# Performance work log

Hardware: AMD Instinct MI355X
Metric: run time of the kernel (lower is better)

The kernel has to match this reference:

```python
import jax, jax.numpy as jnp
import numpy as np

DIM = 1024
HEADS = 8
HEAD_DIM = DIM // HEADS
TAU = HEAD_DIM ** 0.5
BS, SEQ = 1, 2048


def setup_inputs() -> dict:
    key = jax.random.key(0)
    kq, kk, kv, kb = jax.random.split(key, 4)
    q = jax.random.normal(kq, (BS, SEQ, DIM), jnp.float32)
    k = jax.random.normal(kk, (BS, SEQ, DIM), jnp.float32)
    v = jax.random.normal(kv, (BS, SEQ, DIM), jnp.float32)
    Wi_w = jnp.zeros((HEADS, 3 * DIM), jnp.float32)
    Wi_b = 0.1 * jax.random.normal(kb, (HEADS,), jnp.float32)
    Wf_w = jnp.zeros((HEADS, 3 * DIM), jnp.float32)
    Wf_b = jnp.linspace(3.0, 6.0, HEADS, dtype=jnp.float32)  # equidistant_bias_init(3, 6)
    gn_w = jnp.ones((DIM,), jnp.float32)
    gn_b = jnp.zeros((DIM,), jnp.float32)
    return {"q": q, "k": k, "v": v, "Wi_w": Wi_w, "Wi_b": Wi_b,
            "Wf_w": Wf_w, "Wf_b": Wf_b, "gn_w": gn_w, "gn_b": gn_b}


def reference(q, k, v, Wi_w, Wi_b, Wf_w, Wf_b, gn_w, gn_b):
    bs, seq, dim = q.shape
    gate_in = jnp.concatenate([q, k, v], axis=-1)                    # [b, s, 3d]
    itilde = jnp.einsum('bsd,hd->bhs', gate_in, Wi_w) + Wi_b[None, :, None]
    ftilde = jnp.einsum('bsd,hd->bhs', gate_in, Wf_w) + Wf_b[None, :, None]

    # Decay matrix: F_act[i,j] = sum_{t=j+1..i} logsigmoid(ftilde_t), lower-tri else -inf
    csum = jnp.cumsum(jax.nn.log_sigmoid(ftilde), axis=-1)           # [b, h, s]
    Fmat = csum[..., :, None] - csum[..., None, :]                   # [b, h, s, s]
    mask = jnp.tril(jnp.ones((seq, seq), dtype=bool))
    F_act = jnp.where(mask, Fmat, -jnp.inf)

    Dtilde = F_act + itilde[..., None, :]                            # add input gate along j
    max_d = jnp.max(Dtilde, axis=-1, keepdims=True)
    D = jnp.exp(Dtilde - max_d)                                      # stabilized decay weights

    qh = q.reshape(bs, seq, HEADS, HEAD_DIM).transpose(0, 2, 1, 3)
    kh = k.reshape(bs, seq, HEADS, HEAD_DIM).transpose(0, 2, 1, 3)
    vh = v.reshape(bs, seq, HEADS, HEAD_DIM).transpose(0, 2, 1, 3)

    Ctilde = jnp.einsum('bhid,bhjd->bhij', qh, kh) * D / TAU
    maxit = jnp.maximum(jnp.abs(jnp.sum(Ctilde, axis=-1, keepdims=True)), jnp.exp(-max_d))
    Htilde = jnp.einsum('bhij,bhjd->bhid', Ctilde, vh) / (maxit + 1e-6)

    # GroupNorm(HEADS groups) over dim, applied per token
    x = Htilde.transpose(0, 2, 1, 3).reshape(bs * seq, HEADS, HEAD_DIM)
    mean = jnp.mean(x, axis=-1, keepdims=True)
    var = jnp.var(x, axis=-1, keepdims=True)
    xn = (x - mean) / jnp.sqrt(var + 1e-5)
    out = xn.reshape(bs * seq, DIM) * gn_w + gn_b
    return out.reshape(bs, seq, DIM)
```

## Files before the change

kernel.cpp:

```cpp
#include <hip/hip_runtime.h>
#include <math.h>

#define SEQ 2048
#define NH 8
#define HD 128
#define DIMF 1024
#define LOG2E 1.4426950408889634f
#define INVTAU 0.08838834764831845f

typedef __attribute__((ext_vector_type(8))) short bf16x8;
typedef __attribute__((ext_vector_type(8))) unsigned short us8;
typedef __attribute__((ext_vector_type(4))) float f32x4;

__device__ float g_itacc[NH*SEQ];
__device__ float g_ftacc[NH*SEQ];
__device__ float g_aL[NH*SEQ];
__device__ float g_cmL[NH*SEQ];
__device__ float g_en[NH*SEQ];
__device__ unsigned short g_Qb[NH*SEQ*HD];
__device__ unsigned short g_Kb[NH*SEQ*HD];
__device__ unsigned short g_Vb[NH*SEQ*HD];
__device__ unsigned short g_Vt[NH*HD*SEQ];
__device__ unsigned short g_Wb[16*3072];
__device__ float g_Opart[640*64*128];
__device__ float g_Spart[640*64];

__device__ __forceinline__ unsigned short f2bf(float x) {
  unsigned u = __float_as_uint(x);
  u += 0x7fffu + ((u >> 16) & 1u);
  return (unsigned short)(u >> 16);
}

__global__ __launch_bounds__(256) void convert_kernel(const float* __restrict__ q,
                                                      const float* __restrict__ k,
                                                      const float* __restrict__ v,
                                                      const float* __restrict__ Wi,
                                                      const float* __restrict__ Wf) {
  const int bid = blockIdx.x;
  if (bid < 6144) {
    const int s = bid & 2047;
    const int t = bid >> 11;
    const float* src = (t == 0) ? q : (t == 1) ? k : v;
    unsigned short* dst = (t == 0) ? g_Qb : (t == 1) ? g_Kb : g_Vb;
    const int c = threadIdx.x * 4;
    const float4 f = *(const float4*)(src + s*DIMF + c);
    const int h = c >> 7, d = c & 127;
    ushort4 u;
    u.x = f2bf(f.x); u.y = f2bf(f.y); u.z = f2bf(f.z); u.w = f2bf(f.w);
    *(ushort4*)(dst + (h*SEQ + s)*HD + d) = u;
  } else {
    const int gid = (bid - 6144) * 256 + threadIdx.x;
    const int e4 = gid * 4;
    const int p = e4 / 3072;
    const int c = e4 % 3072;
    const float* src = (p < 8) ? (Wi + p*3072 + c) : (Wf + (p-8)*3072 + c);
    const float4 f = *(const float4*)src;
    ushort4 u;
    u.x = f2bf(f.x); u.y = f2bf(f.y); u.z = f2bf(f.z); u.w = f2bf(f.w);
    *(ushort4*)(g_Wb + p*3072 + c) = u;
  }
}

__global__ __launch_bounds__(256) void vtrans_kernel() {
  __shared__ __align__(16) unsigned short Ts[64*72];
  const int h  = blockIdx.x;
  const int s0 = blockIdx.y * 64;
  const int d0 = blockIdx.z * 64;
  const int t = threadIdx.x;
  {
    const int sr = t >> 2;
    const int c  = (t & 3) * 16;
    const unsigned short* src = g_Vb + (h*SEQ + s0 + sr)*HD + d0 + c;
    *(us8*)&Ts[sr*72 + c]     = *(const us8*)&src[0];
    *(us8*)&Ts[sr*72 + c + 8] = *(const us8*)&src[8];
  }
  __syncthreads();
  {
    const int w = t >> 6, l = t & 63;
    unsigned short outv[16];
    #pragma unroll
    for (int j = 0; j < 16; ++j) outv[j] = Ts[(w*16 + j)*72 + l];
    unsigned short* dst = g_Vt + (h*HD + d0 + l)*SEQ + s0 + w*16;
    *(us8*)&dst[0] = *(us8*)&outv[0];
    *(us8*)&dst[8] = *(us8*)&outv[8];
  }
}

__global__ __launch_bounds__(256) void gates_kernel() {
  __shared__ f32x4 red[4][64];
  const int tid = threadIdx.x;
  const int wave = tid >> 6, lane = tid & 63;
  const int q4 = lane >> 4, l16 = lane & 15;
  const int s0 = blockIdx.x * 16;
  f32x4 acc = {0.f, 0.f, 0.f, 0.f};
  #pragma unroll 8
  for (int ks = wave*24; ks < wave*24 + 24; ++ks) {
    const int k0 = ks*32 + q4*8;
    const int tsel = k0 >> 10;
    const int rem = k0 & 1023;
    const int hh = rem >> 7, dd = rem & 127;
    const unsigned short* base = (tsel == 0) ? g_Qb : (tsel == 1) ? g_Kb : g_Vb;
    const bf16x8 a = *(const bf16x8*)&base[(hh*SEQ + s0 + l16)*HD + dd];
    const bf16x8 b = *(const bf16x8*)&g_Wb[l16*3072 + k0];
    acc = __builtin_amdgcn_mfma_f32_16x16x32_bf16(a, b, acc, 0, 0, 0);
  }
  red[wave][lane] = acc;
  __syncthreads();
  if (wave == 0) {
    f32x4 s = red[0][lane];
    #pragma unroll
    for (int w = 1; w < 4; ++w) s += red[w][lane];
    #pragma unroll
    for (int r = 0; r < 4; ++r) {
      const int sg = s0 + 4*q4 + r;
      if (l16 < 8) g_itacc[l16*SEQ + sg] = s[r];
      else         g_ftacc[(l16-8)*SEQ + sg] = s[r];
    }
  }
}

__global__ __launch_bounds__(256) void scan_kernel(const float* __restrict__ Wi_b,
                                                   const float* __restrict__ Wf_b) {
  __shared__ float Wsum[4];
  __shared__ float Wmax[4];
  const int h = blockIdx.x;
  const int t = threadIdx.x;
  const int wave = t >> 6, lane = t & 63;
  const float ib = Wi_b[h];
  const float fb = Wf_b[h];
  const int base = h*SEQ + t*8;

  float it[8], ft[8];
  *(float4*)&it[0] = *(const float4*)&g_itacc[base];
  *(float4*)&it[4] = *(const float4*)&g_itacc[base+4];
  *(float4*)&ft[0] = *(const float4*)&g_ftacc[base];
  *(float4*)&ft[4] = *(const float4*)&g_ftacc[base+4];

  float cs[8];
  float run = 0.f;
  #pragma unroll
  for (int j = 0; j < 8; ++j) {
    const float f = ft[j] + fb;
    const float ls = fminf(f, 0.f) - log1pf(expf(-fabsf(f)));
    run += ls;
    cs[j] = run;
  }
  float x = run;
  #pragma unroll
  for (int off = 1; off < 64; off <<= 1) {
    const float tv = __shfl_up(x, off, 64);
    if (lane >= off) x += tv;
  }
  const float wexcl = x - run;
  if (lane == 63) Wsum[wave] = x;
  __syncthreads();
  float boff = 0.f;
  #pragma unroll
  for (int w = 0; w < 4; ++w) if (w < wave) boff += Wsum[w];
  const float cbase = boff + wexcl;

  float a[8], am[8], csum[8];
  float m = -__builtin_inff();
  #pragma unroll
  for (int j = 0; j < 8; ++j) {
    csum[j] = cbase + cs[j];
    a[j] = (it[j] + ib) - csum[j];
    m = fmaxf(m, a[j]);
    am[j] = m;
  }
  float y = m;
  #pragma unroll
  for (int off = 1; off < 64; off <<= 1) {
    const float tv = __shfl_up(y, off, 64);
    if (lane >= off) y = fmaxf(y, tv);
  }
  float e = __shfl_up(y, 1, 64);
  if (lane == 0) e = -__builtin_inff();
  if (lane == 63) Wmax[wave] = y;
  __syncthreads();
  float bmax = -__builtin_inff();
  #pragma unroll
  for (int w = 0; w < 4; ++w) if (w < wave) bmax = fmaxf(bmax, Wmax[w]);
  const float pre = fmaxf(bmax, e);

  float oa[8], ocm[8], oen[8];
  #pragma unroll
  for (int j = 0; j < 8; ++j) {
    const float cm = fmaxf(pre, am[j]);
    oa[j]  = a[j] * LOG2E;
    ocm[j] = cm * LOG2E;
    oen[j] = expf(-(csum[j] + cm));
  }
  *(float4*)&g_aL[base]    = *(float4*)&oa[0];
  *(float4*)&g_aL[base+4]  = *(float4*)&oa[4];
  *(float4*)&g_cmL[base]   = *(float4*)&ocm[0];
  *(float4*)&g_cmL[base+4] = *(float4*)&ocm[4];
  *(float4*)&g_en[base]    = *(float4*)&oen[0];
  *(float4*)&g_en[base+4]  = *(float4*)&oen[4];
}

__global__ __launch_bounds__(256, 2) void attn1_kernel() {
  __shared__ __align__(16) unsigned short Ks[64*136];
  __shared__ __align__(16) unsigned short Ps[64*72];
  __shared__ __align__(16) unsigned short Vt[128*72];
  __shared__ float Sred[64][2];

  const int h = blockIdx.x;
  const int y = blockIdx.y;
  int g, s0g;
  if      (y < 8)  { g = 0; s0g = 0;  }
  else if (y < 24) { g = 1; s0g = 8;  }
  else if (y < 48) { g = 2; s0g = 24; }
  else             { g = 3; s0g = 48; }
  const int rel = y - s0g;
  const int iT  = 8*g + rel/(g+1);
  const int ch  = rel - (rel/(g+1))*(g+1);
  const int slot = h*80 + y;
  const int i0 = iT*64;
  const int jt0 = ch*8;
  const int jt1 = (jt0 + 8 < iT + 1) ? (jt0 + 8) : (iT + 1);

  const int tid = threadIdx.x;
  const int wave = tid >> 6;
  const int lane = tid & 63;
  const int q4 = lane >> 4;
  const int l16 = lane & 15;
  const int wr = wave >> 1;
  const int wc = wave & 1;

  bf16x8 qa[2][4];
  {
    const unsigned short* Qg = g_Qb + (h*SEQ + i0 + 32*wr + l16)*HD;
    #pragma unroll
    for (int tr = 0; tr < 2; ++tr)
      #pragma unroll
      for (int ks = 0; ks < 4; ++ks)
        qa[tr][ks] = *(const bf16x8*)&Qg[tr*16*HD + ks*32 + q4*8];
  }

  float cmv[2][4];
  #pragma unroll
  for (int tr = 0; tr < 2; ++tr)
    #pragma unroll
    for (int r = 0; r < 4; ++r)
      cmv[tr][r] = g_cmL[h*SEQ + i0 + 32*wr + 16*tr + 4*q4 + r];

  f32x4 accH[2][4];
  float rs[2][4];
  const f32x4 fzero = {0.f, 0.f, 0.f, 0.f};
  #pragma unroll
  for (int tr = 0; tr < 2; ++tr) {
    #pragma unroll
    for (int tc = 0; tc < 4; ++tc) accH[tr][tc] = fzero;
    #pragma unroll
    for (int r = 0; r < 4; ++r) rs[tr][r] = 0.f;
  }

  const int r0 = tid >> 4;
  const int c8 = (tid & 15) * 8;
  const int dK = tid >> 1;
  const int cV = (tid & 1) * 32;

  const unsigned short* Kgh = g_Kb + h*SEQ*HD;
  const unsigned short* Vgh = g_Vt + h*HD*SEQ;

  us8 Kr[4], Vr[4];
  {
    const unsigned short* kp = Kgh + jt0*64*HD;
    const unsigned short* vp = Vgh + jt0*64;
    #pragma unroll
    for (int i = 0; i < 4; ++i) Kr[i] = *(const us8*)&kp[(r0 + 16*i)*HD + c8];
    #pragma unroll
    for (int j = 0; j < 4; ++j) Vr[j] = *(const us8*)&vp[dK*SEQ + cV + 8*j];
  }

  for (int jt = jt0; jt < jt1; ++jt) {
    const int j0 = jt*64;
    __syncthreads();
    #pragma unroll
    for (int i = 0; i < 4; ++i) *(us8*)&Ks[(r0 + 16*i)*136 + c8] = Kr[i];
    #pragma unroll
    for (int j = 0; j < 4; ++j) *(us8*)&Vt[dK*72 + cV + 8*j] = Vr[j];
    float aLv[2];
    aLv[0] = g_aL[h*SEQ + j0 + 32*wc + l16];
    aLv[1] = g_aL[h*SEQ + j0 + 32*wc + 16 + l16];
    __syncthreads();

    if (jt + 1 < jt1) {
      const unsigned short* kp = Kgh + (j0 + 64)*HD;
      const unsigned short* vp = Vgh + (j0 + 64);
      #pragma unroll
      for (int i = 0; i < 4; ++i) Kr[i] = *(const us8*)&kp[(r0 + 16*i)*HD + c8];
      #pragma unroll
      for (int j = 0; j < 4; ++j) Vr[j] = *(const us8*)&vp[dK*SEQ + cV + 8*j];
    }

    f32x4 c00 = fzero, c01 = fzero, c10 = fzero, c11 = fzero;
    #pragma unroll
    for (int ks = 0; ks < 4; ++ks) {
      const int ko = ks*32 + q4*8;
      const bf16x8 b0 = *(const bf16x8*)&Ks[(32*wc      + l16)*136 + ko];
      const bf16x8 b1 = *(const bf16x8*)&Ks[(32*wc + 16 + l16)*136 + ko];
      c00 = __builtin_amdgcn_mfma_f32_16x16x32_bf16(qa[0][ks], b0, c00, 0, 0, 0);
      c01 = __builtin_amdgcn_mfma_f32_16x16x32_bf16(qa[0][ks], b1, c01, 0, 0, 0);
      c10 = __builtin_amdgcn_mfma_f32_16x16x32_bf16(qa[1][ks], b0, c10, 0, 0, 0);
      c11 = __builtin_amdgcn_mfma_f32_16x16x32_bf16(qa[1][ks], b1, c11, 0, 0, 0);
    }

    const bool diag = (jt == iT);
    #pragma unroll
    for (int tr = 0; tr < 2; ++tr) {
      #pragma unroll
      for (int tc = 0; tc < 2; ++tc) {
        const f32x4 cc = tr ? (tc ? c11 : c10) : (tc ? c01 : c00);
        const int jg = j0 + 32*wc + 16*tc + l16;
        #pragma unroll
        for (int r = 0; r < 4; ++r) {
          const int rloc = 32*wr + 16*tr + 4*q4 + r;
          const int ig = i0 + rloc;
          const float w = exp2f(aLv[tc] - cmv[tr][r]) * INVTAU;
          float p = cc[r] * w;
          if (diag && (jg > ig)) p = 0.f;
          rs[tr][r] += p;
          Ps[rloc*72 + 32*wc + 16*tc + l16] = f2bf(p);
        }
      }
    }
    __syncthreads();

    #pragma unroll
    for (int ks = 0; ks < 2; ++ks) {
      const int ko = ks*32 + q4*8;
      const bf16x8 p0 = *(const bf16x8*)&Ps[(32*wr      + l16)*72 + ko];
      const bf16x8 p1 = *(const bf16x8*)&Ps[(32*wr + 16 + l16)*72 + ko];
      #pragma unroll
      for (int tc = 0; tc < 4; ++tc) {
        const bf16x8 vb = *(const bf16x8*)&Vt[(64*wc + 16*tc + l16)*72 + ko];
        accH[0][tc] = __builtin_amdgcn_mfma_f32_16x16x32_bf16(p0, vb, accH[0][tc], 0, 0, 0);
        accH[1][tc] = __builtin_amdgcn_mfma_f32_16x16x32_bf16(p1, vb, accH[1][tc], 0, 0, 0);
      }
    }
  }

  #pragma unroll
  for (int tr = 0; tr < 2; ++tr)
    #pragma unroll
    for (int r = 0; r < 4; ++r) {
      float t = rs[tr][r];
      t += __shfl_xor(t, 1, 16);
      t += __shfl_xor(t, 2, 16);
      t += __shfl_xor(t, 4, 16);
      t += __shfl_xor(t, 8, 16);
      rs[tr][r] = t;
    }
  if (l16 == 0) {
    #pragma unroll
    for (int tr = 0; tr < 2; ++tr)
      #pragma unroll
      for (int r = 0; r < 4; ++r)
        Sred[32*wr + 16*tr + 4*q4 + r][wc] = rs[tr][r];
  }
  __syncthreads();

  if (tid < 64) g_Spart[slot*64 + tid] = Sred[tid][0] + Sred[tid][1];

  float* Ob = g_Opart + slot*(64*128);
  #pragma unroll
  for (int tr = 0; tr < 2; ++tr)
    #pragma unroll
    for (int r = 0; r < 4; ++r) {
      const int rloc = 32*wr + 16*tr + 4*q4 + r;
      #pragma unroll
      for (int tc = 0; tc < 4; ++tc)
        Ob[rloc*128 + 64*wc + 16*tc + l16] = accH[tr][tc][r];
    }
}

__global__ __launch_bounds__(256) void reduce_kernel(const float* __restrict__ gnw,
                                                     const float* __restrict__ gnb,
                                                     float* __restrict__ out) {
  const int h  = blockIdx.x;
  const int iT = blockIdx.y;
  const int t  = threadIdx.x;
  const int r  = t >> 2;
  const int qd = t & 3;
  const int qq = iT >> 3;
  const int nch = qq + 1;
  const int slot0 = h*80 + iT + 4*qq*(qq-1) + qq*(iT & 7);

  float acc[32];
  #pragma unroll
  for (int e = 0; e < 32; ++e) acc[e] = 0.f;
  float S = 0.f;
  for (int c = 0; c < nch; ++c) {
    const float* Ob = g_Opart + (slot0 + c)*(64*128) + r*128 + qd*32;
    #pragma unroll
    for (int kk = 0; kk < 8; ++kk) {
      const float4 f = *(const float4*)&Ob[kk*4];
      acc[kk*4+0] += f.x; acc[kk*4+1] += f.y; acc[kk*4+2] += f.z; acc[kk*4+3] += f.w;
    }
    S += g_Spart[(slot0 + c)*64 + r];
  }

  const float en = g_en[h*SEQ + iT*64 + r];
  const float sc = 1.f / (fmaxf(fabsf(S), en) + 1e-6f);
  float s1 = 0.f, s2 = 0.f;
  #pragma unroll
  for (int e = 0; e < 32; ++e) {
    const float xv = acc[e] * sc;
    acc[e] = xv;
    s1 += xv;
    s2 += xv * xv;
  }
  s1 += __shfl_xor(s1, 1, 4); s2 += __shfl_xor(s2, 1, 4);
  s1 += __shfl_xor(s1, 2, 4); s2 += __shfl_xor(s2, 2, 4);
  const float mean = s1 * (1.f/128.f);
  const float var  = s2 * (1.f/128.f) - mean*mean;
  const float rstd = rsqrtf(var + 1e-5f);

  const float* gw = gnw + h*HD + qd*32;
  const float* gb = gnb + h*HD + qd*32;
  float* op = out + (iT*64 + r)*DIMF + h*HD + qd*32;
  #pragma unroll
  for (int kk = 0; kk < 8; ++kk) {
    const float4 w4 = *(const float4*)&gw[kk*4];
    const float4 b4 = *(const float4*)&gb[kk*4];
    float4 o;
    o.x = (acc[kk*4+0] - mean) * rstd * w4.x + b4.x;
    o.y = (acc[kk*4+1] - mean) * rstd * w4.y + b4.y;
    o.z = (acc[kk*4+2] - mean) * rstd * w4.z + b4.z;
    o.w = (acc[kk*4+3] - mean) * rstd * w4.w + b4.w;
    *(float4*)&op[kk*4] = o;
  }
}

extern "C" void kernel_launch(void* const* d_in, const int* in_sizes, int n_in,
                              void* d_out, int out_size, void* d_ws, size_t ws_size,
                              hipStream_t stream) {
  (void)in_sizes; (void)n_in; (void)out_size; (void)d_ws; (void)ws_size;
  const float* q    = (const float*)d_in[0];
  const float* k    = (const float*)d_in[1];
  const float* v    = (const float*)d_in[2];
  const float* Wi_w = (const float*)d_in[3];
  const float* Wi_b = (const float*)d_in[4];
  const float* Wf_w = (const float*)d_in[5];
  const float* Wf_b = (const float*)d_in[6];
  const float* gnw  = (const float*)d_in[7];
  const float* gnb  = (const float*)d_in[8];
  float* out = (float*)d_out;

  convert_kernel<<<dim3(6192), 256, 0, stream>>>(q, k, v, Wi_w, Wf_w);
  vtrans_kernel<<<dim3(NH, SEQ/64, HD/64), 256, 0, stream>>>();
  gates_kernel<<<dim3(128), 256, 0, stream>>>();
  scan_kernel<<<dim3(NH), 256, 0, stream>>>(Wi_b, Wf_b);
  attn1_kernel<<<dim3(NH, 80), 256, 0, stream>>>();
  reduce_kernel<<<dim3(NH, SEQ/64), 256, 0, stream>>>(gnw, gnb, out);
}
```

Before: 156.9 us.

## Rewrite attention kernel with register-only 32x32 MFMA and permlane P exchange

The attention kernel drops its shared-memory staging of K, V and P. It computes S transposed with 32x32x16 MFMAs, with each wave loading its K and V fragments straight from global memory. It then converts P to bf16 in registers with permlane32_swap to feed the PV MFMA, and splits the j range across wave pairs, merging the two partial outputs through shared memory at the end. This removes the per-tile barriers and LDS round trips. In exchange each wave issues redundant global loads with no explicit prefetch, and the grid order becomes head-major.

```diff
diff --git a/kernel.cpp b/kernel.cpp
--- a/kernel.cpp
+++ b/kernel.cpp
@@ -11,6 +11,7 @@
 typedef __attribute__((ext_vector_type(8))) short bf16x8;
 typedef __attribute__((ext_vector_type(8))) unsigned short us8;
 typedef __attribute__((ext_vector_type(4))) float f32x4;
+typedef __attribute__((ext_vector_type(16))) float f32x16;
 
 __device__ float g_itacc[NH*SEQ];
 __device__ float g_ftacc[NH*SEQ];
@@ -29,6 +30,10 @@
   unsigned u = __float_as_uint(x);
   u += 0x7fffu + ((u >> 16) & 1u);
   return (unsigned short)(u >> 16);
+}
+
+__device__ __forceinline__ unsigned packbf(float lo, float hi) {
+  return (unsigned)f2bf(lo) | ((unsigned)f2bf(hi) << 16);
 }
 
 __global__ __launch_bounds__(256) void convert_kernel(const float* __restrict__ q,
@@ -200,13 +205,11 @@
 }
 
 __global__ __launch_bounds__(256, 2) void attn1_kernel() {
-  __shared__ __align__(16) unsigned short Ks[64*136];
-  __shared__ __align__(16) unsigned short Ps[64*72];
-  __shared__ __align__(16) unsigned short Vt[128*72];
+  __shared__ float Osum[2][32][128];
   __shared__ float Sred[64][2];
 
-  const int h = blockIdx.x;
-  const int y = blockIdx.y;
+  const int y = blockIdx.x;
+  const int h = blockIdx.y;
   int g, s0g;
   if      (y < 8)  { g = 0; s0g = 0;  }
   else if (y < 24) { g = 1; s0g = 8;  }
@@ -220,160 +223,109 @@
   const int jt0 = ch*8;
   const int jt1 = (jt0 + 8 < iT + 1) ? (jt0 + 8) : (iT + 1);
 
-  const int tid = threadIdx.x;
+  const int tid  = threadIdx.x;
   const int wave = tid >> 6;
   const int lane = tid & 63;
-  const int q4 = lane >> 4;
-  const int l16 = lane & 15;
-  const int wr = wave >> 1;
-  const int wc = wave & 1;
-
-  bf16x8 qa[2][4];
+  const int l31  = lane & 31;
+  const int hi   = lane >> 5;
+  const int wr   = wave >> 1;
+  const int wc   = wave & 1;
+
+  bf16x8 qf[8];
   {
-    const unsigned short* Qg = g_Qb + (h*SEQ + i0 + 32*wr + l16)*HD;
-    #pragma unroll
-    for (int tr = 0; tr < 2; ++tr)
-      #pragma unroll
-      for (int ks = 0; ks < 4; ++ks)
-        qa[tr][ks] = *(const bf16x8*)&Qg[tr*16*HD + ks*32 + q4*8];
-  }
-
-  float cmv[2][4];
-  #pragma unroll
-  for (int tr = 0; tr < 2; ++tr)
-    #pragma unroll
-    for (int r = 0; r < 4; ++r)
-      cmv[tr][r] = g_cmL[h*SEQ + i0 + 32*wr + 16*tr + 4*q4 + r];
-
-  f32x4 accH[2][4];
-  float rs[2][4];
-  const f32x4 fzero = {0.f, 0.f, 0.f, 0.f};
-  #pragma unroll
-  for (int tr = 0; tr < 2; ++tr) {
-    #pragma unroll
-    for (int tc = 0; tc < 4; ++tc) accH[tr][tc] = fzero;
-    #pragma unroll
-    for (int r = 0; r < 4; ++r) rs[tr][r] = 0.f;
-  }
-
-  const int r0 = tid >> 4;
-  const int c8 = (tid & 15) * 8;
-  const int dK = tid >> 1;
-  const int cV = (tid & 1) * 32;
-
-  const unsigned short* Kgh = g_Kb + h*SEQ*HD;
-  const unsigned short* Vgh = g_Vt + h*HD*SEQ;
-
-  us8 Kr[4], Vr[4];
-  {
-    const unsigned short* kp = Kgh + jt0*64*HD;
-    const unsigned short* vp = Vgh + jt0*64;
-    #pragma unroll
-    for (int i = 0; i < 4; ++i) Kr[i] = *(const us8*)&kp[(r0 + 16*i)*HD + c8];
-    #pragma unroll
-    for (int j = 0; j < 4; ++j) Vr[j] = *(const us8*)&vp[dK*SEQ + cV + 8*j];
-  }
+    const unsigned short* Qg = g_Qb + (h*SEQ + i0 + 32*wr + l31)*HD + hi*8;
+    #pragma unroll
+    for (int ks = 0; ks < 8; ++ks) qf[ks] = *(const bf16x8*)&Qg[ks*16];
+  }
+  const float cm = g_cmL[h*SEQ + i0 + 32*wr + l31];
+  const int   ig = i0 + 32*wr + l31;
+
+  f32x16 acc[4];
+  #pragma unroll
+  for (int td = 0; td < 4; ++td)
+    #pragma unroll
+    for (int e = 0; e < 16; ++e) acc[td][e] = 0.f;
+  float rs_sum = 0.f;
+
+  const unsigned short* Kg  = g_Kb + (h*SEQ + 32*wc + l31)*HD + hi*8;
+  const unsigned short* Vg  = g_Vt + (h*HD + l31)*SEQ + 32*wc + hi*8;
+  const float*          aLg = g_aL + h*SEQ + 32*wc + 4*hi;
 
   for (int jt = jt0; jt < jt1; ++jt) {
     const int j0 = jt*64;
-    __syncthreads();
-    #pragma unroll
-    for (int i = 0; i < 4; ++i) *(us8*)&Ks[(r0 + 16*i)*136 + c8] = Kr[i];
-    #pragma unroll
-    for (int j = 0; j < 4; ++j) *(us8*)&Vt[dK*72 + cV + 8*j] = Vr[j];
-    float aLv[2];
-    aLv[0] = g_aL[h*SEQ + j0 + 32*wc + l16];
-    aLv[1] = g_aL[h*SEQ + j0 + 32*wc + 16 + l16];
-    __syncthreads();
-
-    if (jt + 1 < jt1) {
-      const unsigned short* kp = Kgh + (j0 + 64)*HD;
-      const unsigned short* vp = Vgh + (j0 + 64);
+    bf16x8 kf[8];
+    #pragma unroll
+    for (int ks = 0; ks < 8; ++ks) kf[ks] = *(const bf16x8*)&Kg[j0*HD + ks*16];
+    float4 aLq[4];
+    #pragma unroll
+    for (int rq = 0; rq < 4; ++rq) aLq[rq] = *(const float4*)&aLg[j0 + 8*rq];
+
+    f32x16 a0, a1;
+    #pragma unroll
+    for (int e = 0; e < 16; ++e) { a0[e] = 0.f; a1[e] = 0.f; }
+    #pragma unroll
+    for (int ks = 0; ks < 8; ks += 2) {
+      a0 = __builtin_amdgcn_mfma_f32_32x32x16_bf16(kf[ks],   qf[ks],   a0, 0, 0, 0);
+      a1 = __builtin_amdgcn_mfma_f32_32x32x16_bf16(kf[ks+1], qf[ks+1], a1, 0, 0, 0);
+    }
+
+    const bool diag = (jt == iT);
+    const int jbase = j0 + 32*wc + 4*hi;
+
+    #pragma unroll
+    for (int ph = 0; ph < 2; ++ph) {
+      float pv[8];
       #pragma unroll
-      for (int i = 0; i < 4; ++i) Kr[i] = *(const us8*)&kp[(r0 + 16*i)*HD + c8];
+      for (int rr = 0; rr < 8; ++rr) {
+        const int r  = 8*ph + rr;
+        const int rq = r >> 2;
+        const float aL = ((const float*)&aLq[rq])[r & 3];
+        float p = (a0[r] + a1[r]) * (exp2f(aL - cm) * INVTAU);
+        const int jg = jbase + 8*rq + (r & 3);
+        if (diag && jg > ig) p = 0.f;
+        rs_sum += p;
+        pv[rr] = p;
+      }
+      const unsigned w0 = packbf(pv[0], pv[1]);
+      const unsigned w1 = packbf(pv[2], pv[3]);
+      const unsigned w2 = packbf(pv[4], pv[5]);
+      const unsigned w3 = packbf(pv[6], pv[7]);
+      const auto s0 = __builtin_amdgcn_permlane32_swap(w0, w2, false, false);
+      const auto s1 = __builtin_amdgcn_permlane32_swap(w1, w3, false, false);
+      union { unsigned u[4]; bf16x8 v; } fr;
+      fr.u[0] = s0[0]; fr.u[1] = s1[0]; fr.u[2] = s0[1]; fr.u[3] = s1[1];
       #pragma unroll
-      for (int j = 0; j < 4; ++j) Vr[j] = *(const us8*)&vp[dK*SEQ + cV + 8*j];
-    }
-
-    f32x4 c00 = fzero, c01 = fzero, c10 = fzero, c11 = fzero;
-    #pragma unroll
-    for (int ks = 0; ks < 4; ++ks) {
-      const int ko = ks*32 + q4*8;
-      const bf16x8 b0 = *(const bf16x8*)&Ks[(32*wc      + l16)*136 + ko];
-      const bf16x8 b1 = *(const bf16x8*)&Ks[(32*wc + 16 + l16)*136 + ko];
-      c00 = __builtin_amdgcn_mfma_f32_16x16x32_bf16(qa[0][ks], b0, c00, 0, 0, 0);
-      c01 = __builtin_amdgcn_mfma_f32_16x16x32_bf16(qa[0][ks], b1, c01, 0, 0, 0);
-      c10 = __builtin_amdgcn_mfma_f32_16x16x32_bf16(qa[1][ks], b0, c10, 0, 0, 0);
-      c11 = __builtin_amdgcn_mfma_f32_16x16x32_bf16(qa[1][ks], b1, c11, 0, 0, 0);
-    }
-
-    const bool diag = (jt == iT);
-    #pragma unroll
-    for (int tr = 0; tr < 2; ++tr) {
-      #pragma unroll
-      for (int tc = 0; tc < 2; ++tc) {
-        const f32x4 cc = tr ? (tc ? c11 : c10) : (tc ? c01 : c00);
-        const int jg = j0 + 32*wc + 16*tc + l16;
-        #pragma unroll
-        for (int r = 0; r < 4; ++r) {
-          const int rloc = 32*wr + 16*tr + 4*q4 + r;
-          const int ig = i0 + rloc;
-          const float w = exp2f(aLv[tc] - cmv[tr][r]) * INVTAU;
-          float p = cc[r] * w;
-          if (diag && (jg > ig)) p = 0.f;
-          rs[tr][r] += p;
-          Ps[rloc*72 + 32*wc + 16*tc + l16] = f2bf(p);
-        }
+      for (int td = 0; td < 4; ++td) {
+        const bf16x8 vb = *(const bf16x8*)&Vg[(32*td)*SEQ + j0 + 16*ph];
+        acc[td] = __builtin_amdgcn_mfma_f32_32x32x16_bf16(fr.v, vb, acc[td], 0, 0, 0);
       }
     }
-    __syncthreads();
-
-    #pragma unroll
-    for (int ks = 0; ks < 2; ++ks) {
-      const int ko = ks*32 + q4*8;
-      const bf16x8 p0 = *(const bf16x8*)&Ps[(32*wr      + l16)*72 + ko];
-      const bf16x8 p1 = *(const bf16x8*)&Ps[(32*wr + 16 + l16)*72 + ko];
+  }
+
+  rs_sum += __shfl_xor(rs_sum, 32, 64);
+  if (hi == 0) Sred[32*wr + l31][wc] = rs_sum;
+
+  if (wc == 0) {
+    #pragma unroll
+    for (int td = 0; td < 4; ++td)
       #pragma unroll
-      for (int tc = 0; tc < 4; ++tc) {
-        const bf16x8 vb = *(const bf16x8*)&Vt[(64*wc + 16*tc + l16)*72 + ko];
-        accH[0][tc] = __builtin_amdgcn_mfma_f32_16x16x32_bf16(p0, vb, accH[0][tc], 0, 0, 0);
-        accH[1][tc] = __builtin_amdgcn_mfma_f32_16x16x32_bf16(p1, vb, accH[1][tc], 0, 0, 0);
+      for (int r = 0; r < 16; ++r) {
+        const int row = (r & 3) + 8*(r >> 2) + 4*hi;
+        Osum[wr][row][32*td + l31] = acc[td][r];
       }
-    }
-  }
-
-  #pragma unroll
-  for (int tr = 0; tr < 2; ++tr)
-    #pragma unroll
-    for (int r = 0; r < 4; ++r) {
-      float t = rs[tr][r];
-      t += __shfl_xor(t, 1, 16);
-      t += __shfl_xor(t, 2, 16);
-      t += __shfl_xor(t, 4, 16);
-      t += __shfl_xor(t, 8, 16);
-      rs[tr][r] = t;
-    }
-  if (l16 == 0) {
-    #pragma unroll
-    for (int tr = 0; tr < 2; ++tr)
+  }
+  __syncthreads();
+  if (wc == 1) {
+    float* Ob = g_Opart + slot*(64*128);
+    #pragma unroll
+    for (int td = 0; td < 4; ++td)
       #pragma unroll
-      for (int r = 0; r < 4; ++r)
-        Sred[32*wr + 16*tr + 4*q4 + r][wc] = rs[tr][r];
-  }
-  __syncthreads();
-
+      for (int r = 0; r < 16; ++r) {
+        const int row = (r & 3) + 8*(r >> 2) + 4*hi;
+        Ob[(32*wr + row)*128 + 32*td + l31] = acc[td][r] + Osum[wr][row][32*td + l31];
+      }
+  }
   if (tid < 64) g_Spart[slot*64 + tid] = Sred[tid][0] + Sred[tid][1];
-
-  float* Ob = g_Opart + slot*(64*128);
-  #pragma unroll
-  for (int tr = 0; tr < 2; ++tr)
-    #pragma unroll
-    for (int r = 0; r < 4; ++r) {
-      const int rloc = 32*wr + 16*tr + 4*q4 + r;
-      #pragma unroll
-      for (int tc = 0; tc < 4; ++tc)
-        Ob[rloc*128 + 64*wc + 16*tc + l16] = accH[tr][tc][r];
-    }
 }
 
 __global__ __launch_bounds__(256) void reduce_kernel(const float* __restrict__ gnw,
@@ -453,6 +405,6 @@
   vtrans_kernel<<<dim3(NH, SEQ/64, HD/64), 256, 0, stream>>>();
   gates_kernel<<<dim3(128), 256, 0, stream>>>();
   scan_kernel<<<dim3(NH), 256, 0, stream>>>(Wi_b, Wf_b);
-  attn1_kernel<<<dim3(NH, 80), 256, 0, stream>>>();
+  attn1_kernel<<<dim3(80, NH), 256, 0, stream>>>();
   reduce_kernel<<<dim3(NH, SEQ/64), 256, 0, stream>>>(gnw, gnb, out);
 }
```

Measured after the change: 172.9 us. 10.2% more time.
